# Kernel optimization log

Measured on AMD Instinct MI355X. Metric: run time of the kernel, lower is better.

Reference implementation:

```python
import jax, jax.numpy as jnp
import numpy as np

GROUP_SIZE = 32
OUT_FEATURES = 4096
IN_FEATURES = 4096


def _unpack_3bit(p):
    # p: [..., 3] uint8 -> [..., 8] 3-bit values in [0, 7]
    b0, b1, b2 = p[..., 0], p[..., 1], p[..., 2]
    v0 = b0 & 7
    v1 = (b0 >> 3) & 7
    v2 = ((b0 >> 6) & 3) | ((b1 & 1) << 2)
    v3 = (b1 >> 1) & 7
    v4 = (b1 >> 4) & 7
    v5 = ((b1 >> 7) & 1) | ((b2 & 3) << 1)
    v6 = (b2 >> 2) & 7
    v7 = (b2 >> 5) & 7
    return jnp.stack([v0, v1, v2, v3, v4, v5, v6, v7], axis=-1)


def _block_dequantize_3bit(packed, normalization, group_size=GROUP_SIZE):
    # packed: [n_groups, group_size*3//8] int8, normalization: [n_groups, 1]
    p = packed.astype(jnp.uint8).reshape(-1, group_size // 8, 3)
    q = _unpack_3bit(p).reshape(-1, group_size).astype(jnp.float32)
    n = normalization.astype(jnp.float32)  # [n_groups, 1]
    x_norm = q / 7.0
    return (x_norm * (2.0 * n) - n).reshape(-1)


def setup_inputs() -> dict:
    key = jax.random.key(0)
    k1, k2, k3, k4 = jax.random.split(key, 4)
    n_groups = OUT_FEATURES * IN_FEATURES // GROUP_SIZE
    packed_cols = GROUP_SIZE * 3 // 8
    x = jax.random.normal(k1, (2, 2048, IN_FEATURES), dtype=jnp.float32)
    weight_q3 = jax.random.randint(k2, (n_groups, packed_cols), 0, 256, dtype=jnp.int32).astype(jnp.int8)
    weight_norm = jax.random.uniform(k3, (n_groups, 1), dtype=jnp.float32, minval=0.05, maxval=1.0)
    bias = jax.random.normal(k4, (OUT_FEATURES,), dtype=jnp.float32) * 0.02
    return {"x": x, "weight_q3": weight_q3, "weight_norm": weight_norm, "bias": bias}


def reference(x, weight_q3, weight_norm, bias):
    # Dequantize 3-bit packed weights to fp32 [out, in], then F.linear.
    w = _block_dequantize_3bit(weight_q3, weight_norm).reshape(OUT_FEATURES, IN_FEATURES)
    return jnp.einsum('bsi,oi->bso', x, w) + bias
```

## Files before the change

### kernel.cpp

```cpp
#include <hip/hip_runtime.h>
#include <hip/hip_bf16.h>
#include <stdint.h>

#define OUTF 4096
#define INF  4096
#define MROWS 4096
#define GS 32

typedef __attribute__((ext_vector_type(8))) __bf16 bf16x8;
typedef __attribute__((ext_vector_type(4))) float f32x4;

__device__ inline void gload_lds16(const void* g, void* l) {
    __builtin_amdgcn_global_load_lds(
        (const __attribute__((address_space(1))) void*)g,
        (__attribute__((address_space(3))) void*)l, 16, 0, 0);
}

__device__ inline void load_group_bits(const int* __restrict__ wq, int gid,
                                       uint64_t& lo, uint64_t& hi) {
    const int4* p = (const int4*)(wq + (size_t)gid * 12);
    int4 A = p[0], B = p[1], C = p[2];
    uint32_t d0 = (uint32_t)(A.x & 255) | ((uint32_t)(A.y & 255) << 8) |
                  ((uint32_t)(A.z & 255) << 16) | ((uint32_t)(A.w & 255) << 24);
    uint32_t d1 = (uint32_t)(B.x & 255) | ((uint32_t)(B.y & 255) << 8) |
                  ((uint32_t)(B.z & 255) << 16) | ((uint32_t)(B.w & 255) << 24);
    uint32_t d2 = (uint32_t)(C.x & 255) | ((uint32_t)(C.y & 255) << 8) |
                  ((uint32_t)(C.z & 255) << 16) | ((uint32_t)(C.w & 255) << 24);
    lo = (uint64_t)d0 | ((uint64_t)d1 << 32);
    hi = (uint64_t)d1 | ((uint64_t)d2 << 32);
}

__global__ void prep_kernel(const float* __restrict__ x, __bf16* __restrict__ xb,
                            const int* __restrict__ wq, const float* __restrict__ wn,
                            __bf16* __restrict__ wb) {
    const int bid = blockIdx.x;
    if (bid < 8192) {
        int i = bid * 256 + threadIdx.x;
        const f32x4* xp = (const f32x4*)x;
        f32x4 a = xp[2 * i], b = xp[2 * i + 1];
        bf16x8 v = { (__bf16)a[0], (__bf16)a[1], (__bf16)a[2], (__bf16)a[3],
                     (__bf16)b[0], (__bf16)b[1], (__bf16)b[2], (__bf16)b[3] };
        ((bf16x8*)xb)[i] = v;
    } else {
        int gid = (bid - 8192) * 256 + threadIdx.x;
        uint64_t lo, hi;
        load_group_bits(wq, gid, lo, hi);
        float nrm = wn[gid];
        float c2 = nrm * (2.0f / 7.0f), c1 = -nrm;
        bf16x8 o[4];
#pragma unroll
        for (int j = 0; j < 32; ++j) {
            uint32_t q = (j <= 20) ? (uint32_t)((lo >> (3 * j)) & 7)
                                   : (uint32_t)((hi >> (3 * j - 32)) & 7);
            o[j >> 3][j & 7] = (__bf16)((float)q * c2 + c1);
        }
        bf16x8* outp = (bf16x8*)(wb + (size_t)gid * 32);
        outp[0] = o[0]; outp[1] = o[1]; outp[2] = o[2]; outp[3] = o[3];
    }
}


#define VMCNTQ(N) asm volatile("s_waitcnt vmcnt(" #N ")" ::: "memory")
#define BARR() do { asm volatile("" ::: "memory"); __builtin_amdgcn_s_barrier(); \
                    asm volatile("" ::: "memory"); } while (0)

#define STAGE3(SOFF, SKT) do { \
    gload_lds16(pa0 + (SKT) * 32, lds + (SOFF) + tid * 16); \
    gload_lds16(pa1 + (SKT) * 32, lds + (SOFF) + 8192 + tid * 16); \
    gload_lds16(pb0 + (SKT) * 32, lds + (SOFF) + 16384 + tid * 16); \
} while (0)

#define RD(ROFF) do { \
    _Pragma("unroll") \
    for (int m_ = 0; m_ < 4; ++m_) \
        af[m_] = *(const bf16x8*)(lds + (ROFF) + (wr * 64 + m_ * 16 + row16) * 64 + swl); \
    _Pragma("unroll") \
    for (int n_ = 0; n_ < 4; ++n_) \
        bf[n_] = *(const bf16x8*)(lds + (ROFF) + 16384 + (wc * 64 + n_ * 16 + row16) * 64 + swl); \
} while (0)

#define MFMA16() do { \
    __builtin_amdgcn_s_setprio(1); \
    _Pragma("unroll") \
    for (int m_ = 0; m_ < 4; ++m_) \
        _Pragma("unroll") \
        for (int n_ = 0; n_ < 4; ++n_) \
            acc[m_][n_] = __builtin_amdgcn_mfma_f32_16x16x32_bf16( \
                af[m_], bf[n_], acc[m_][n_], 0, 0, 0); \
    __builtin_amdgcn_s_setprio(0); \
} while (0)

#define ROT(V) do { (V) += 24576; if ((V) == 3 * 24576) (V) = 0; } while (0)

__global__ __launch_bounds__(512, 4) void gemm3_kernel(
    const __bf16* __restrict__ xb, const __bf16* __restrict__ wb,
    const float* __restrict__ bias, float* __restrict__ out) {
    __shared__ __align__(16) unsigned char lds[3 * 24576];

    const int tid = threadIdx.x;
    const int lane = tid & 63, wid = tid >> 6;
    const int wr = wid >> 1, wc = wid & 1;
    const int row16 = lane & 15, kq = lane >> 4;
    const int swl = (kq ^ ((row16 & 3) ^ ((row16 >> 2) & 3))) * 16;

    const int bid = blockIdx.x;
    const int wg = (bid & 7) * 64 + (bid >> 3);
    const int bm = wg >> 5, bn = wg & 31;

    const int ar0 = tid >> 2;
    const int ac0 = ((tid & 3) ^ ((ar0 & 3) ^ ((ar0 >> 2) & 3))) * 8;
    const int ar1 = (tid + 512) >> 2;
    const int ac1 = ((tid & 3) ^ ((ar1 & 3) ^ ((ar1 >> 2) & 3))) * 8;
    const __bf16* pa0 = xb + (size_t)(bm * 256 + ar0) * INF + ac0;
    const __bf16* pa1 = xb + (size_t)(bm * 256 + ar1) * INF + ac1;
    const __bf16* pb0 = wb + (size_t)(bn * 128 + ar0) * INF + ac0;

    f32x4 acc[4][4] = {};
    bf16x8 af[4], bf[4];

    STAGE3(0, 0);
    STAGE3(24576, 1);

    int roff = 0, soff = 2 * 24576;
    for (int kt = 0; kt < 126; ++kt) {
        VMCNTQ(3);
        BARR();
        STAGE3(soff, kt + 2);
        RD(roff);
        MFMA16();
        ROT(roff); ROT(soff);
    }
    VMCNTQ(3);
    BARR();
    RD(roff);
    MFMA16();
    ROT(roff);
    VMCNTQ(0);
    BARR();
    RD(roff);
    MFMA16();

#pragma unroll
    for (int n = 0; n < 4; ++n) {
        const int col = bn * 128 + wc * 64 + n * 16 + row16;
        const float bv = bias[col];
#pragma unroll
        for (int m = 0; m < 4; ++m) {
            const int rbase = bm * 256 + wr * 64 + m * 16 + kq * 4;
#pragma unroll
            for (int j = 0; j < 4; ++j)
                out[(size_t)(rbase + j) * OUTF + col] = acc[m][n][j] + bv;
        }
    }
}

__global__ __launch_bounds__(256, 2) void gemm_fb_kernel(
    const float* __restrict__ x, const int* __restrict__ wq,
    const float* __restrict__ wn, const float* __restrict__ bias,
    float* __restrict__ out) {
    __shared__ __align__(16) unsigned char lAraw[128 * 128];
    __shared__ __align__(16) unsigned char lBraw[128 * 128];

    const int tid = threadIdx.x;
    const int lane = tid & 63, wid = tid >> 6;
    const int wr = wid >> 1, wc = wid & 1;
    const int bn = blockIdx.x, bm = blockIdx.y;
    const int row16 = lane & 15, kq = lane >> 4;

    f32x4 acc[4][4] = {};

    int aoff[4], boff[4];
#pragma unroll
    for (int m = 0; m < 4; ++m) {
        int r = wr * 64 + m * 16 + row16;
        aoff[m] = r * 128 + ((kq * 16) ^ ((r & 7) << 4));
    }
#pragma unroll
    for (int n = 0; n < 4; ++n) {
        int r = wc * 64 + n * 16 + row16;
        boff[n] = r * 128 + ((kq * 16) ^ ((r & 7) << 4));
    }

    for (int kt = 0; kt < INF / 64; ++kt) {
        __syncthreads();
#pragma unroll
        for (int it = 0; it < 4; ++it) {
            int row = it * 32 + (tid >> 3), c = tid & 7;
            const f32x4* xp = (const f32x4*)(x + (size_t)(bm * 128 + row) * INF + kt * 64 + c * 8);
            f32x4 a0 = xp[0], a1 = xp[1];
            bf16x8 v = { (__bf16)a0[0], (__bf16)a0[1], (__bf16)a0[2], (__bf16)a0[3],
                         (__bf16)a1[0], (__bf16)a1[1], (__bf16)a1[2], (__bf16)a1[3] };
            *(bf16x8*)(lAraw + row * 128 + ((c * 16) ^ ((row & 7) << 4))) = v;
        }
        {
            int row = tid >> 1, gi = tid & 1;
            int gid = (bn * 128 + row) * (INF / GS) + kt * 2 + gi;
            uint64_t lo, hi;
            load_group_bits(wq, gid, lo, hi);
            float nrm = wn[gid];
            float c2 = nrm * (2.0f / 7.0f), c1 = -nrm;
            bf16x8 o[4];
#pragma unroll
            for (int j = 0; j < 32; ++j) {
                uint32_t q = (j <= 20) ? (uint32_t)((lo >> (3 * j)) & 7)
                                       : (uint32_t)((hi >> (3 * j - 32)) & 7);
                o[j >> 3][j & 7] = (__bf16)((float)q * c2 + c1);
            }
            unsigned swz = (row & 7) << 4;
#pragma unroll
            for (int c4 = 0; c4 < 4; ++c4)
                *(bf16x8*)(lBraw + row * 128 + ((gi * 64 + c4 * 16) ^ swz)) = o[c4];
        }
        __syncthreads();

#pragma unroll
        for (int kk = 0; kk < 2; ++kk) {
            bf16x8 afr[4], bfr[4];
#pragma unroll
            for (int m = 0; m < 4; ++m)
                afr[m] = *(const bf16x8*)(lAraw + (aoff[m] ^ (kk * 64)));
#pragma unroll
            for (int n = 0; n < 4; ++n)
                bfr[n] = *(const bf16x8*)(lBraw + (boff[n] ^ (kk * 64)));
#pragma unroll
            for (int m = 0; m < 4; ++m)
#pragma unroll
                for (int n = 0; n < 4; ++n)
                    acc[m][n] = __builtin_amdgcn_mfma_f32_16x16x32_bf16(afr[m], bfr[n], acc[m][n], 0, 0, 0);
        }
    }

#pragma unroll
    for (int n = 0; n < 4; ++n) {
        int col = bn * 128 + wc * 64 + n * 16 + row16;
        float bv = bias[col];
#pragma unroll
        for (int m = 0; m < 4; ++m) {
            int rbase = bm * 128 + wr * 64 + m * 16 + kq * 4;
#pragma unroll
            for (int j = 0; j < 4; ++j)
                out[(size_t)(rbase + j) * OUTF + col] = acc[m][n][j] + bv;
        }
    }
}

extern "C" void kernel_launch(void* const* d_in, const int* in_sizes, int n_in,
                              void* d_out, int out_size, void* d_ws, size_t ws_size,
                              hipStream_t stream) {
    const float* x    = (const float*)d_in[0];
    const int*   wq   = (const int*)d_in[1];
    const float* wn   = (const float*)d_in[2];
    const float* bias = (const float*)d_in[3];
    float* out = (float*)d_out;

    const size_t xb_bytes = (size_t)MROWS * INF * 2;
    const size_t wb_bytes = (size_t)OUTF * INF * 2;
    if (ws_size >= xb_bytes + wb_bytes) {
        __bf16* xb = (__bf16*)d_ws;
        __bf16* wb = (__bf16*)((char*)d_ws + xb_bytes);
        prep_kernel<<<8192 + (OUTF * INF / GS) / 256, 256, 0, stream>>>(x, xb, wq, wn, wb);
        gemm3_kernel<<<(MROWS / 256) * (OUTF / 128), 512, 0, stream>>>(xb, wb, bias, out);
    } else {
        gemm_fb_kernel<<<dim3(OUTF / 128, MROWS / 128), 256, 0, stream>>>(x, wq, wn, bias, out);
    }
}
```

Before: 163.6 us.

## Restructure GEMM to 256x256 tiles with A fragments loaded directly from global

Replaces the 256x128 triple-buffered GEMM with a 256x256 tile per workgroup. Only the weight (B) tile goes through double-buffered LDS, while each wave reads its A fragments straight from global memory into registers. The larger tile doubles the accumulators per wave and halves the number of workgroups. The aim is to cut LDS traffic and improve reuse per byte loaded. The costs are more register pressure (occupancy bound drops from 4 to 2 blocks), uncoalesced global A reads, a full vmcnt(0) wait each iteration, and a pipeline that is only two stages deep.

After: 232.7 us. 42.2% more time.

```diff
diff --git a/kernel.cpp b/kernel.cpp
--- a/kernel.cpp
+++ b/kernel.cpp
@@ -60,89 +60,80 @@
 }
 
 
-#define VMCNTQ(N) asm volatile("s_waitcnt vmcnt(" #N ")" ::: "memory")
+#define VMCNT0() asm volatile("s_waitcnt vmcnt(0)" ::: "memory")
 #define BARR() do { asm volatile("" ::: "memory"); __builtin_amdgcn_s_barrier(); \
                     asm volatile("" ::: "memory"); } while (0)
 
-#define STAGE3(SOFF, SKT) do { \
-    gload_lds16(pa0 + (SKT) * 32, lds + (SOFF) + tid * 16); \
-    gload_lds16(pa1 + (SKT) * 32, lds + (SOFF) + 8192 + tid * 16); \
-    gload_lds16(pb0 + (SKT) * 32, lds + (SOFF) + 16384 + tid * 16); \
-} while (0)
-
-#define RD(ROFF) do { \
-    _Pragma("unroll") \
-    for (int m_ = 0; m_ < 4; ++m_) \
-        af[m_] = *(const bf16x8*)(lds + (ROFF) + (wr * 64 + m_ * 16 + row16) * 64 + swl); \
-    _Pragma("unroll") \
-    for (int n_ = 0; n_ < 4; ++n_) \
-        bf[n_] = *(const bf16x8*)(lds + (ROFF) + 16384 + (wc * 64 + n_ * 16 + row16) * 64 + swl); \
-} while (0)
-
-#define MFMA16() do { \
-    __builtin_amdgcn_s_setprio(1); \
-    _Pragma("unroll") \
-    for (int m_ = 0; m_ < 4; ++m_) \
-        _Pragma("unroll") \
-        for (int n_ = 0; n_ < 4; ++n_) \
-            acc[m_][n_] = __builtin_amdgcn_mfma_f32_16x16x32_bf16( \
-                af[m_], bf[n_], acc[m_][n_], 0, 0, 0); \
-    __builtin_amdgcn_s_setprio(0); \
-} while (0)
-
-#define ROT(V) do { (V) += 24576; if ((V) == 3 * 24576) (V) = 0; } while (0)
-
-__global__ __launch_bounds__(512, 4) void gemm3_kernel(
+__global__ __launch_bounds__(512, 2) void gemmA_kernel(
     const __bf16* __restrict__ xb, const __bf16* __restrict__ wb,
     const float* __restrict__ bias, float* __restrict__ out) {
-    __shared__ __align__(16) unsigned char lds[3 * 24576];
+    __shared__ __align__(16) unsigned char lds[2 * 32768];
 
     const int tid = threadIdx.x;
     const int lane = tid & 63, wid = tid >> 6;
     const int wr = wid >> 1, wc = wid & 1;
     const int row16 = lane & 15, kq = lane >> 4;
-    const int swl = (kq ^ ((row16 & 3) ^ ((row16 >> 2) & 3))) * 16;
 
     const int bid = blockIdx.x;
-    const int wg = (bid & 7) * 64 + (bid >> 3);
-    const int bm = wg >> 5, bn = wg & 31;
-
-    const int ar0 = tid >> 2;
-    const int ac0 = ((tid & 3) ^ ((ar0 & 3) ^ ((ar0 >> 2) & 3))) * 8;
-    const int ar1 = (tid + 512) >> 2;
-    const int ac1 = ((tid & 3) ^ ((ar1 & 3) ^ ((ar1 >> 2) & 3))) * 8;
-    const __bf16* pa0 = xb + (size_t)(bm * 256 + ar0) * INF + ac0;
-    const __bf16* pa1 = xb + (size_t)(bm * 256 + ar1) * INF + ac1;
-    const __bf16* pb0 = wb + (size_t)(bn * 128 + ar0) * INF + ac0;
-
-    f32x4 acc[4][4] = {};
-    bf16x8 af[4], bf[4];
-
-    STAGE3(0, 0);
-    STAGE3(24576, 1);
-
-    int roff = 0, soff = 2 * 24576;
-    for (int kt = 0; kt < 126; ++kt) {
-        VMCNTQ(3);
+    const int wg = (bid & 7) * 32 + (bid >> 3);
+    const int bn = wg & 15, bm = wg >> 4;
+
+    const int srow = tid >> 3;
+    const int schunk = (tid & 7) ^ (srow & 7);
+    const __bf16* pb = wb + (size_t)(bn * 256 + srow) * INF + schunk * 8;
+
+    const __bf16* pa = xb + (size_t)(bm * 256 + wr * 64 + row16) * INF + kq * 8;
+
+    f32x4 acc[4][8] = {};
+    bf16x8 a[4][2];
+
+    int boff[8][2];
+#pragma unroll
+    for (int n = 0; n < 8; ++n) {
+        const int R = wc * 128 + n * 16 + row16;
+#pragma unroll
+        for (int kk = 0; kk < 2; ++kk)
+            boff[n][kk] = R * 128 + (((kk * 4 + kq) * 16) ^ ((R & 7) << 4));
+    }
+
+#pragma unroll
+    for (int j = 0; j < 4; ++j)
+        gload_lds16(pb + (size_t)j * 64 * INF, lds + j * 8192 + tid * 16);
+    VMCNT0();
+    BARR();
+
+    for (int kt = 0; kt < INF / 64; ++kt) {
+        const int rb = kt & 1, sb = rb ^ 1;
+        if (kt < INF / 64 - 1) {
+#pragma unroll
+            for (int j = 0; j < 4; ++j)
+                gload_lds16(pb + (size_t)j * 64 * INF + (kt + 1) * 64,
+                            lds + sb * 32768 + j * 8192 + tid * 16);
+        }
+#pragma unroll
+        for (int m = 0; m < 4; ++m)
+#pragma unroll
+            for (int kk = 0; kk < 2; ++kk)
+                a[m][kk] = *(const bf16x8*)(pa + (size_t)m * 16 * INF + kt * 64 + kk * 32);
+#pragma unroll
+        for (int n = 0; n < 8; ++n) {
+            bf16x8 b0 = *(const bf16x8*)(lds + rb * 32768 + boff[n][0]);
+            bf16x8 b1 = *(const bf16x8*)(lds + rb * 32768 + boff[n][1]);
+            __builtin_amdgcn_s_setprio(1);
+#pragma unroll
+            for (int m = 0; m < 4; ++m) {
+                acc[m][n] = __builtin_amdgcn_mfma_f32_16x16x32_bf16(a[m][0], b0, acc[m][n], 0, 0, 0);
+                acc[m][n] = __builtin_amdgcn_mfma_f32_16x16x32_bf16(a[m][1], b1, acc[m][n], 0, 0, 0);
+            }
+            __builtin_amdgcn_s_setprio(0);
+        }
+        VMCNT0();
         BARR();
-        STAGE3(soff, kt + 2);
-        RD(roff);
-        MFMA16();
-        ROT(roff); ROT(soff);
-    }
-    VMCNTQ(3);
-    BARR();
-    RD(roff);
-    MFMA16();
-    ROT(roff);
-    VMCNTQ(0);
-    BARR();
-    RD(roff);
-    MFMA16();
-
-#pragma unroll
-    for (int n = 0; n < 4; ++n) {
-        const int col = bn * 128 + wc * 64 + n * 16 + row16;
+    }
+
+#pragma unroll
+    for (int n = 0; n < 8; ++n) {
+        const int col = bn * 256 + wc * 128 + n * 16 + row16;
         const float bv = bias[col];
 #pragma unroll
         for (int m = 0; m < 4; ++m) {
@@ -259,7 +250,7 @@
         __bf16* xb = (__bf16*)d_ws;
         __bf16* wb = (__bf16*)((char*)d_ws + xb_bytes);
         prep_kernel<<<8192 + (OUTF * INF / GS) / 256, 256, 0, stream>>>(x, xb, wq, wn, wb);
-        gemm3_kernel<<<(MROWS / 256) * (OUTF / 128), 512, 0, stream>>>(xb, wb, bias, out);
+        gemmA_kernel<<<(MROWS / 256) * (OUTF / 256), 512, 0, stream>>>(xb, wb, bias, out);
     } else {
         gemm_fb_kernel<<<dim3(OUTF / 128, MROWS / 128), 256, 0, stream>>>(x, wq, wn, bias, out);
     }
```
